# Performance work log

Hardware: AMD Instinct MI355X
Metric: run time of the kernel (lower is better)

Reference implementation:

```python
import jax, jax.numpy as jnp
import numpy as np


def setup_inputs() -> dict:
    key = jax.random.key(0)
    ks = jax.random.split(key, 6)
    B, Q, K = 4, 512, 1024
    Dq, Dk, Dv, H = 512, 512, 512, 128
    return {
        "queries": jax.random.normal(ks[0], (B, Q, Dq), dtype=jnp.float32),
        "keys": jax.random.normal(ks[1], (B, K, Dk), dtype=jnp.float32),
        "values": jax.random.normal(ks[2], (B, K, Dv), dtype=jnp.float32),
        "W_q": jax.random.normal(ks[3], (Dq, H), dtype=jnp.float32) / np.sqrt(Dq),
        "W_k": jax.random.normal(ks[4], (Dk, H), dtype=jnp.float32) / np.sqrt(Dk),
        "w_v": jax.random.normal(ks[5], (H,), dtype=jnp.float32) / np.sqrt(H),
    }


def reference(queries, keys, values, W_q, W_k, w_v):
    # Additive (Bahdanau) attention.
    q = jnp.einsum("bqd,dh->bqh", queries, W_q)          # [B,Q,H]
    k = jnp.einsum("bkd,dh->bkh", keys, W_k)             # [B,K,H]
    features = jnp.tanh(q[:, :, None, :] + k[:, None, :, :])  # [B,Q,K,H]
    scores = jnp.einsum("bqkh,h->bqk", features, w_v)    # [B,Q,K]
    attn = jax.nn.softmax(scores, axis=-1)               # [B,Q,K]
    return jnp.einsum("bqk,bkv->bqv", attn, values)      # [B,Q,Dv]
```

## Files before the change

kernel.cpp:

```cpp
#include <hip/hip_runtime.h>

#define BB   4
#define QS   512
#define KSZ  1024
#define DD   512
#define HH   128
#define DVV  512

__device__ __forceinline__ float rcp_fast(float x)  { return __builtin_amdgcn_rcpf(x); }
__device__ __forceinline__ float exp2_fast(float x) { return __builtin_amdgcn_exp2f(x); }

__global__ __launch_bounds__(256) void proj_exp_kernel(
    const float* __restrict__ q,  const float* __restrict__ k,
    const float* __restrict__ Wq, const float* __restrict__ Wk,
    float* __restrict__ eq, float* __restrict__ ek, int nq_blocks)
{
    __shared__ float At[16][36];
    __shared__ float Wt[32][128];

    const float* A; const float* W; float* outp; int m0;
    if ((int)blockIdx.x < nq_blocks) {
        A = q;  W = Wq; outp = eq; m0 = blockIdx.x * 16;
    } else {
        A = k;  W = Wk; outp = ek; m0 = (blockIdx.x - nq_blocks) * 16;
    }

    const int tid = threadIdx.x;
    const int h4  = tid & 31;
    const int r   = tid >> 5;

    float4 acc0 = {0.f,0.f,0.f,0.f};
    float4 acc1 = {0.f,0.f,0.f,0.f};

    for (int d0 = 0; d0 < DD; d0 += 32) {
        if (tid < 128) {
            int row = tid >> 3, c4 = tid & 7;
            *(float4*)&At[row][c4 * 4] =
                *(const float4*)&A[(size_t)(m0 + row) * DD + d0 + c4 * 4];
        }
        #pragma unroll
        for (int i = 0; i < 4; i++) {
            int f = tid + i * 256;
            int row = f >> 5, c4 = f & 31;
            *(float4*)&Wt[row][c4 * 4] =
                *(const float4*)&W[(size_t)(d0 + row) * HH + c4 * 4];
        }
        __syncthreads();
        #pragma unroll 4
        for (int kk = 0; kk < 32; kk++) {
            float4 w4 = *(const float4*)&Wt[kk][h4 * 4];
            float a0 = At[r][kk];
            float a1 = At[r + 8][kk];
            acc0.x = fmaf(a0, w4.x, acc0.x); acc0.y = fmaf(a0, w4.y, acc0.y);
            acc0.z = fmaf(a0, w4.z, acc0.z); acc0.w = fmaf(a0, w4.w, acc0.w);
            acc1.x = fmaf(a1, w4.x, acc1.x); acc1.y = fmaf(a1, w4.y, acc1.y);
            acc1.z = fmaf(a1, w4.z, acc1.z); acc1.w = fmaf(a1, w4.w, acc1.w);
        }
        __syncthreads();
    }

    const float C2L = 2.8853900817779268f;
    float4 o0, o1;
    o0.x = exp2_fast(acc0.x * C2L); o0.y = exp2_fast(acc0.y * C2L);
    o0.z = exp2_fast(acc0.z * C2L); o0.w = exp2_fast(acc0.w * C2L);
    o1.x = exp2_fast(acc1.x * C2L); o1.y = exp2_fast(acc1.y * C2L);
    o1.z = exp2_fast(acc1.z * C2L); o1.w = exp2_fast(acc1.w * C2L);
    *(float4*)&outp[(size_t)(m0 + r)     * HH + h4 * 4] = o0;
    *(float4*)&outp[(size_t)(m0 + r + 8) * HH + h4 * 4] = o1;
}

__global__ __launch_bounds__(256) void scores_kernel(
    const float* __restrict__ eq, const float* __restrict__ ek,
    const float* __restrict__ wv, float* __restrict__ sc)
{
    __shared__ float eqs[64][68];
    __shared__ float eks[64][68];
    __shared__ float wvs[HH];

    const int tid = threadIdx.x;
    const int b  = blockIdx.z;
    const int q0 = blockIdx.y * 64;
    const int k0 = blockIdx.x * 64;

    const float* eqb = eq + ((size_t)b * QS  + q0) * HH;
    const float* ekb = ek + ((size_t)b * KSZ + k0) * HH;

    if (tid < 32) *(float4*)&wvs[tid * 4] = *(const float4*)&wv[tid * 4];

    const int tk = tid & 15;
    const int tq = tid >> 4;

    float acc[4][4] = {};

    for (int hc = 0; hc < HH; hc += 64) {
        __syncthreads();
        #pragma unroll
        for (int i = 0; i < 4; i++) {
            int f = tid + i * 256;
            int row = f >> 4, c4 = f & 15;
            *(float4*)&eqs[row][c4 * 4] =
                *(const float4*)&eqb[(size_t)row * HH + hc + c4 * 4];
            *(float4*)&eks[row][c4 * 4] =
                *(const float4*)&ekb[(size_t)row * HH + hc + c4 * 4];
        }
        __syncthreads();

        for (int h0 = 0; h0 < 64; h0 += 4) {
            float4 wv4 = *(const float4*)&wvs[hc + h0];
            float4 eq4[4], ek4[4];
            #pragma unroll
            for (int j = 0; j < 4; j++) {
                eq4[j] = *(const float4*)&eqs[tq + 16 * j][h0];
                ek4[j] = *(const float4*)&eks[tk + 16 * j][h0];
            }
            #pragma unroll
            for (int jq = 0; jq < 4; jq++) {
                #pragma unroll
                for (int jk = 0; jk < 4; jk++) {
                    acc[jq][jk] = fmaf(wv4.x, rcp_fast(fmaf(eq4[jq].x, ek4[jk].x, 1.0f)), acc[jq][jk]);
                    acc[jq][jk] = fmaf(wv4.y, rcp_fast(fmaf(eq4[jq].y, ek4[jk].y, 1.0f)), acc[jq][jk]);
                    acc[jq][jk] = fmaf(wv4.z, rcp_fast(fmaf(eq4[jq].z, ek4[jk].z, 1.0f)), acc[jq][jk]);
                    acc[jq][jk] = fmaf(wv4.w, rcp_fast(fmaf(eq4[jq].w, ek4[jk].w, 1.0f)), acc[jq][jk]);
                }
            }
        }
    }

    float* scb = sc + ((size_t)b * QS + q0) * KSZ + k0;
    #pragma unroll
    for (int jq = 0; jq < 4; jq++)
        #pragma unroll
        for (int jk = 0; jk < 4; jk++)
            scb[(size_t)(tq + 16 * jq) * KSZ + tk + 16 * jk] = acc[jq][jk];
}

__global__ __launch_bounds__(256) void pv_gemm_kernel(
    const float* __restrict__ sc, const float* __restrict__ val,
    float* __restrict__ outp)
{
    __shared__ float As[2][32][68];
    __shared__ float Bs[2][32][68];
    __shared__ float rsum[64];

    const int tid = threadIdx.x;
    const int b  = blockIdx.z;
    const int m0 = blockIdx.y * 64;
    const int n0 = blockIdx.x * 64;

    const float* scb = sc  + ((size_t)b * QS + m0) * KSZ;
    const float* vb  = val + (size_t)b * KSZ * DVV + n0;

    const int ar = tid >> 3;
    const int ak = (tid & 7) * 4;
    const int bk = tid >> 4;
    const int bn = (tid & 15) * 4;

    const float CN = -2.8853900817779268f;

    float4 ea0, ea1, vv0, vv1;
    float rs0 = 0.f, rs1 = 0.f;

    {
        float4 r0 = *(const float4*)&scb[(size_t)ar * KSZ + ak];
        float4 r1 = *(const float4*)&scb[(size_t)(ar + 32) * KSZ + ak];
        ea0.x = exp2_fast(r0.x * CN); ea0.y = exp2_fast(r0.y * CN);
        ea0.z = exp2_fast(r0.z * CN); ea0.w = exp2_fast(r0.w * CN);
        ea1.x = exp2_fast(r1.x * CN); ea1.y = exp2_fast(r1.y * CN);
        ea1.z = exp2_fast(r1.z * CN); ea1.w = exp2_fast(r1.w * CN);
        vv0 = *(const float4*)&vb[(size_t)bk * DVV + bn];
        vv1 = *(const float4*)&vb[(size_t)(bk + 16) * DVV + bn];
    }
    As[0][ak + 0][ar] = ea0.x; As[0][ak + 1][ar] = ea0.y;
    As[0][ak + 2][ar] = ea0.z; As[0][ak + 3][ar] = ea0.w;
    As[0][ak + 0][ar + 32] = ea1.x; As[0][ak + 1][ar + 32] = ea1.y;
    As[0][ak + 2][ar + 32] = ea1.z; As[0][ak + 3][ar + 32] = ea1.w;
    *(float4*)&Bs[0][bk][bn]      = vv0;
    *(float4*)&Bs[0][bk + 16][bn] = vv1;
    rs0 += ea0.x + ea0.y + ea0.z + ea0.w;
    rs1 += ea1.x + ea1.y + ea1.z + ea1.w;

    const int tm = (tid & 15) * 4;
    const int tn = (tid >> 4) * 4;
    float acc[4][4] = {};

    for (int s = 0; s < 32; s++) {
        __syncthreads();
        const int buf = s & 1;
        if (s < 31) {
            const int k0 = (s + 1) * 32;
            float4 r0 = *(const float4*)&scb[(size_t)ar * KSZ + k0 + ak];
            float4 r1 = *(const float4*)&scb[(size_t)(ar + 32) * KSZ + k0 + ak];
            ea0.x = exp2_fast(r0.x * CN); ea0.y = exp2_fast(r0.y * CN);
            ea0.z = exp2_fast(r0.z * CN); ea0.w = exp2_fast(r0.w * CN);
            ea1.x = exp2_fast(r1.x * CN); ea1.y = exp2_fast(r1.y * CN);
            ea1.z = exp2_fast(r1.z * CN); ea1.w = exp2_fast(r1.w * CN);
            vv0 = *(const float4*)&vb[(size_t)(k0 + bk) * DVV + bn];
            vv1 = *(const float4*)&vb[(size_t)(k0 + bk + 16) * DVV + bn];
        }
        #pragma unroll
        for (int kk = 0; kk < 32; kk++) {
            float4 a4 = *(const float4*)&As[buf][kk][tm];
            float4 b4 = *(const float4*)&Bs[buf][kk][tn];
            acc[0][0] = fmaf(a4.x, b4.x, acc[0][0]); acc[0][1] = fmaf(a4.x, b4.y, acc[0][1]);
            acc[0][2] = fmaf(a4.x, b4.z, acc[0][2]); acc[0][3] = fmaf(a4.x, b4.w, acc[0][3]);
            acc[1][0] = fmaf(a4.y, b4.x, acc[1][0]); acc[1][1] = fmaf(a4.y, b4.y, acc[1][1]);
            acc[1][2] = fmaf(a4.y, b4.z, acc[1][2]); acc[1][3] = fmaf(a4.y, b4.w, acc[1][3]);
            acc[2][0] = fmaf(a4.z, b4.x, acc[2][0]); acc[2][1] = fmaf(a4.z, b4.y, acc[2][1]);
            acc[2][2] = fmaf(a4.z, b4.z, acc[2][2]); acc[2][3] = fmaf(a4.z, b4.w, acc[2][3]);
            acc[3][0] = fmaf(a4.w, b4.x, acc[3][0]); acc[3][1] = fmaf(a4.w, b4.y, acc[3][1]);
            acc[3][2] = fmaf(a4.w, b4.z, acc[3][2]); acc[3][3] = fmaf(a4.w, b4.w, acc[3][3]);
        }
        if (s < 31) {
            const int nb = buf ^ 1;
            As[nb][ak + 0][ar] = ea0.x; As[nb][ak + 1][ar] = ea0.y;
            As[nb][ak + 2][ar] = ea0.z; As[nb][ak + 3][ar] = ea0.w;
            As[nb][ak + 0][ar + 32] = ea1.x; As[nb][ak + 1][ar + 32] = ea1.y;
            As[nb][ak + 2][ar + 32] = ea1.z; As[nb][ak + 3][ar + 32] = ea1.w;
            *(float4*)&Bs[nb][bk][bn]      = vv0;
            *(float4*)&Bs[nb][bk + 16][bn] = vv1;
            rs0 += ea0.x + ea0.y + ea0.z + ea0.w;
            rs1 += ea1.x + ea1.y + ea1.z + ea1.w;
        }
    }

    #pragma unroll
    for (int m = 4; m; m >>= 1) {
        rs0 += __shfl_xor(rs0, m);
        rs1 += __shfl_xor(rs1, m);
    }
    if ((tid & 7) == 0) { rsum[ar] = rs0; rsum[ar + 32] = rs1; }
    __syncthreads();

    float* ob = outp + ((size_t)b * QS + m0) * DVV + n0;
    #pragma unroll
    for (int i = 0; i < 4; i++) {
        float inv = rcp_fast(rsum[tm + i]);
        float4 o;
        o.x = acc[i][0] * inv; o.y = acc[i][1] * inv;
        o.z = acc[i][2] * inv; o.w = acc[i][3] * inv;
        *(float4*)&ob[(size_t)(tm + i) * DVV + tn] = o;
    }
}

extern "C" void kernel_launch(void* const* d_in, const int* in_sizes, int n_in,
                              void* d_out, int out_size, void* d_ws, size_t ws_size,
                              hipStream_t stream)
{
    const float* queries = (const float*)d_in[0];
    const float* keys    = (const float*)d_in[1];
    const float* values  = (const float*)d_in[2];
    const float* Wq      = (const float*)d_in[3];
    const float* Wk      = (const float*)d_in[4];
    const float* wv      = (const float*)d_in[5];
    float* out = (float*)d_out;

    float* eq = (float*)d_ws;
    float* ek = eq + (size_t)BB * QS * HH;
    float* sc = ek + (size_t)BB * KSZ * HH;

    const int nq_blocks = BB * QS / 16;
    const int nk_blocks = BB * KSZ / 16;
    proj_exp_kernel<<<dim3(nq_blocks + nk_blocks), 256, 0, stream>>>(
        queries, keys, Wq, Wk, eq, ek, nq_blocks);

    scores_kernel<<<dim3(KSZ / 64, QS / 64, BB), 256, 0, stream>>>(eq, ek, wv, sc);

    pv_gemm_kernel<<<dim3(DVV / 64, QS / 64, BB), 256, 0, stream>>>(sc, values, out);
}
```

Measured before the change: 171.8 us.

## Split PV GEMM over K slabs with reduction kernel and swizzled LDS

The P·V GEMM is split along the key dimension into 4 slabs. This raises the grid from 256 to 1024 blocks so more of the CUs are busy. Each slab writes unnormalized partial outputs and row sums to workspace, and a new reduce kernel sums them and normalizes. The transposed A tile in LDS also gets an XOR swizzle to cut bank conflicts on the strided stores. The cost is an extra launch and about 16 MB of partial-output traffic through memory.

```diff
diff --git a/kernel.cpp b/kernel.cpp
--- a/kernel.cpp
+++ b/kernel.cpp
@@ -6,6 +6,9 @@
 #define DD   512
 #define HH   128
 #define DVV  512
+
+#define SLABS 4
+#define BKK  (KSZ / SLABS)
 
 __device__ __forceinline__ float rcp_fast(float x)  { return __builtin_amdgcn_rcpf(x); }
 __device__ __forceinline__ float exp2_fast(float x) { return __builtin_amdgcn_exp2f(x); }
@@ -136,24 +139,30 @@
 
 __global__ __launch_bounds__(256) void pv_gemm_kernel(
     const float* __restrict__ sc, const float* __restrict__ val,
-    float* __restrict__ outp)
+    float* __restrict__ part, float* __restrict__ rsp)
 {
     __shared__ float As[2][32][68];
     __shared__ float Bs[2][32][68];
     __shared__ float rsum[64];
 
-    const int tid = threadIdx.x;
-    const int b  = blockIdx.z;
-    const int m0 = blockIdx.y * 64;
-    const int n0 = blockIdx.x * 64;
-
-    const float* scb = sc  + ((size_t)b * QS + m0) * KSZ;
-    const float* vb  = val + (size_t)b * KSZ * DVV + n0;
+    const int tid  = threadIdx.x;
+    const int b    = blockIdx.z >> 2;
+    const int slab = blockIdx.z & 3;
+    const int m0   = blockIdx.y * 64;
+    const int n0   = blockIdx.x * 64;
+    const int kb   = slab * BKK;
+
+    const float* scb = sc  + ((size_t)b * QS + m0) * KSZ + kb;
+    const float* vb  = val + (size_t)b * KSZ * DVV + (size_t)kb * DVV + n0;
 
     const int ar = tid >> 3;
     const int ak = (tid & 7) * 4;
+    const int sA = (ak >> 2) & 3;
     const int bk = tid >> 4;
     const int bn = (tid & 15) * 4;
+
+    const int ca0 = 4 * ((ar >> 2)       ^ sA) + (ar & 3);
+    const int ca1 = 4 * (((ar + 32) >> 2) ^ sA) + (ar & 3);
 
     const float CN = -2.8853900817779268f;
 
@@ -170,23 +179,25 @@
         vv0 = *(const float4*)&vb[(size_t)bk * DVV + bn];
         vv1 = *(const float4*)&vb[(size_t)(bk + 16) * DVV + bn];
     }
-    As[0][ak + 0][ar] = ea0.x; As[0][ak + 1][ar] = ea0.y;
-    As[0][ak + 2][ar] = ea0.z; As[0][ak + 3][ar] = ea0.w;
-    As[0][ak + 0][ar + 32] = ea1.x; As[0][ak + 1][ar + 32] = ea1.y;
-    As[0][ak + 2][ar + 32] = ea1.z; As[0][ak + 3][ar + 32] = ea1.w;
+    As[0][ak + 0][ca0] = ea0.x; As[0][ak + 1][ca0] = ea0.y;
+    As[0][ak + 2][ca0] = ea0.z; As[0][ak + 3][ca0] = ea0.w;
+    As[0][ak + 0][ca1] = ea1.x; As[0][ak + 1][ca1] = ea1.y;
+    As[0][ak + 2][ca1] = ea1.z; As[0][ak + 3][ca1] = ea1.w;
     *(float4*)&Bs[0][bk][bn]      = vv0;
     *(float4*)&Bs[0][bk + 16][bn] = vv1;
     rs0 += ea0.x + ea0.y + ea0.z + ea0.w;
     rs1 += ea1.x + ea1.y + ea1.z + ea1.w;
 
     const int tm = (tid & 15) * 4;
+    const int gm = tid & 15;
     const int tn = (tid >> 4) * 4;
     float acc[4][4] = {};
 
-    for (int s = 0; s < 32; s++) {
+    const int NSTEP = BKK / 32;
+    for (int s = 0; s < NSTEP; s++) {
         __syncthreads();
         const int buf = s & 1;
-        if (s < 31) {
+        if (s < NSTEP - 1) {
             const int k0 = (s + 1) * 32;
             float4 r0 = *(const float4*)&scb[(size_t)ar * KSZ + k0 + ak];
             float4 r1 = *(const float4*)&scb[(size_t)(ar + 32) * KSZ + k0 + ak];
@@ -199,7 +210,7 @@
         }
         #pragma unroll
         for (int kk = 0; kk < 32; kk++) {
-            float4 a4 = *(const float4*)&As[buf][kk][tm];
+            float4 a4 = *(const float4*)&As[buf][kk][4 * (gm ^ ((kk >> 2) & 3))];
             float4 b4 = *(const float4*)&Bs[buf][kk][tn];
             acc[0][0] = fmaf(a4.x, b4.x, acc[0][0]); acc[0][1] = fmaf(a4.x, b4.y, acc[0][1]);
             acc[0][2] = fmaf(a4.x, b4.z, acc[0][2]); acc[0][3] = fmaf(a4.x, b4.w, acc[0][3]);
@@ -210,12 +221,12 @@
             acc[3][0] = fmaf(a4.w, b4.x, acc[3][0]); acc[3][1] = fmaf(a4.w, b4.y, acc[3][1]);
             acc[3][2] = fmaf(a4.w, b4.z, acc[3][2]); acc[3][3] = fmaf(a4.w, b4.w, acc[3][3]);
         }
-        if (s < 31) {
+        if (s < NSTEP - 1) {
             const int nb = buf ^ 1;
-            As[nb][ak + 0][ar] = ea0.x; As[nb][ak + 1][ar] = ea0.y;
-            As[nb][ak + 2][ar] = ea0.z; As[nb][ak + 3][ar] = ea0.w;
-            As[nb][ak + 0][ar + 32] = ea1.x; As[nb][ak + 1][ar + 32] = ea1.y;
-            As[nb][ak + 2][ar + 32] = ea1.z; As[nb][ak + 3][ar + 32] = ea1.w;
+            As[nb][ak + 0][ca0] = ea0.x; As[nb][ak + 1][ca0] = ea0.y;
+            As[nb][ak + 2][ca0] = ea0.z; As[nb][ak + 3][ca0] = ea0.w;
+            As[nb][ak + 0][ca1] = ea1.x; As[nb][ak + 1][ca1] = ea1.y;
+            As[nb][ak + 2][ca1] = ea1.z; As[nb][ak + 3][ca1] = ea1.w;
             *(float4*)&Bs[nb][bk][bn]      = vv0;
             *(float4*)&Bs[nb][bk + 16][bn] = vv1;
             rs0 += ea0.x + ea0.y + ea0.z + ea0.w;
@@ -231,15 +242,35 @@
     if ((tid & 7) == 0) { rsum[ar] = rs0; rsum[ar + 32] = rs1; }
     __syncthreads();
 
-    float* ob = outp + ((size_t)b * QS + m0) * DVV + n0;
+    float* pb = part + (size_t)slab * BB * QS * DVV
+                     + ((size_t)b * QS + m0) * DVV + n0;
     #pragma unroll
     for (int i = 0; i < 4; i++) {
-        float inv = rcp_fast(rsum[tm + i]);
         float4 o;
-        o.x = acc[i][0] * inv; o.y = acc[i][1] * inv;
-        o.z = acc[i][2] * inv; o.w = acc[i][3] * inv;
-        *(float4*)&ob[(size_t)(tm + i) * DVV + tn] = o;
-    }
+        o.x = acc[i][0]; o.y = acc[i][1]; o.z = acc[i][2]; o.w = acc[i][3];
+        *(float4*)&pb[(size_t)(tm + i) * DVV + tn] = o;
+    }
+    if (tid < 64)
+        rsp[slab * (BB * QS) + b * QS + m0 + tid] = rsum[tid];
+}
+
+__global__ __launch_bounds__(256) void reduce_kernel(
+    const float* __restrict__ part, const float* __restrict__ rsp,
+    float* __restrict__ outp)
+{
+    const int i = blockIdx.x * 256 + threadIdx.x;
+    const size_t N4 = (size_t)BB * QS * DVV / 4;
+    const float4* p = (const float4*)part;
+    float4 a = p[i], b = p[i + N4], c = p[i + 2 * N4], d = p[i + 3 * N4];
+    const int bm = i >> 7;
+    float rs = rsp[bm] + rsp[BB * QS + bm] + rsp[2 * BB * QS + bm] + rsp[3 * BB * QS + bm];
+    float inv = rcp_fast(rs);
+    float4 o;
+    o.x = (a.x + b.x + c.x + d.x) * inv;
+    o.y = (a.y + b.y + c.y + d.y) * inv;
+    o.z = (a.z + b.z + c.z + d.z) * inv;
+    o.w = (a.w + b.w + c.w + d.w) * inv;
+    ((float4*)outp)[i] = o;
 }
 
 extern "C" void kernel_launch(void* const* d_in, const int* in_sizes, int n_in,
@@ -254,9 +285,11 @@
     const float* wv      = (const float*)d_in[5];
     float* out = (float*)d_out;
 
-    float* eq = (float*)d_ws;
-    float* ek = eq + (size_t)BB * QS * HH;
-    float* sc = ek + (size_t)BB * KSZ * HH;
+    float* eq   = (float*)d_ws;
+    float* ek   = eq + (size_t)BB * QS * HH;
+    float* sc   = ek + (size_t)BB * KSZ * HH;
+    float* part = sc + (size_t)BB * QS * KSZ;
+    float* rsp  = part + (size_t)SLABS * BB * QS * DVV;
 
     const int nq_blocks = BB * QS / 16;
     const int nk_blocks = BB * KSZ / 16;
@@ -265,5 +298,8 @@
 
     scores_kernel<<<dim3(KSZ / 64, QS / 64, BB), 256, 0, stream>>>(eq, ek, wv, sc);
 
-    pv_gemm_kernel<<<dim3(DVV / 64, QS / 64, BB), 256, 0, stream>>>(sc, values, out);
-}
+    pv_gemm_kernel<<<dim3(DVV / 64, QS / 64, BB * SLABS), 256, 0, stream>>>(
+        sc, values, part, rsp);
+
+    reduce_kernel<<<dim3(BB * QS * DVV / 4 / 256), 256, 0, stream>>>(part, rsp, out);
+}
```

After: 185.8 us. 1.08x slower.
